# Kernel tuning notes

Hardware: AMD Instinct MI355X
Metric: run time of the kernel (lower is better)

## Reference

```python
import jax, jax.numpy as jnp
import numpy as np

N = 4096       # rows (batch * points)
D = 512        # d_model
H = 8          # num_heads


def setup_inputs() -> dict:
    key = jax.random.key(0)
    ks = jax.random.split(key, 11)
    s = 1.0 / np.sqrt(D).astype(np.float32)
    return {
        "x_q": jax.random.normal(ks[0], (N, D), jnp.float32),
        "x_k": jax.random.normal(ks[1], (N, D), jnp.float32),
        "x_v": jax.random.normal(ks[2], (N, D), jnp.float32),
        "Wq": jax.random.normal(ks[3], (D, D), jnp.float32) * s,
        "bq": jax.random.normal(ks[4], (D,), jnp.float32) * s,
        "Wk": jax.random.normal(ks[5], (D, D), jnp.float32) * s,
        "bk": jax.random.normal(ks[6], (D,), jnp.float32) * s,
        "Wv": jax.random.normal(ks[7], (D, D), jnp.float32) * s,
        "bv": jax.random.normal(ks[8], (D,), jnp.float32) * s,
        "Wo": jax.random.normal(ks[9], (D, D), jnp.float32) * s,
        "bo": jax.random.normal(ks[10], (D,), jnp.float32) * s,
    }


def reference(x_q, x_k, x_v, Wq, bq, Wk, bk, Wv, bv, Wo, bo):
    n, d = x_q.shape
    d_k = d // H
    # linear projections
    q = (x_q @ Wq + bq).reshape(n, H, d_k)  # chunk(dim=-1) == head split
    k = (x_k @ Wk + bk).reshape(n, H, d_k)
    v = (x_v @ Wv + bv).reshape(n, H, d_k)
    # channel-wise outer-product attention: scores[n,h,i,j] = q_i * k_j / sqrt(d_k)
    scale = jnp.asarray(1.0 / np.sqrt(d_k), q.dtype)
    scores = q[..., :, None] * k[..., None, :] * scale  # (n, H, d_k, d_k)
    p = jax.nn.softmax(scores, axis=-1)
    # attn output: p @ v over channel axis -> (n, H, d_k)
    x = jnp.einsum('nhij,nhj->nhi', p, v).reshape(n, d)  # head merge (cat dim=-1)
    return (x_q - x) @ Wo + bo
```

## Files before the change

kernel.cpp:

```cpp
#include <hip/hip_runtime.h>
#include <hip/hip_bf16.h>

#define NROWS 4096
#define DMODEL 512
#define NHEAD 8
#define DKH 64
#define ND (NROWS * DMODEL)
#define DD (DMODEL * DMODEL)

typedef unsigned short u16;
typedef __attribute__((ext_vector_type(8))) short short8;
typedef __attribute__((ext_vector_type(4))) float floatx4;

__device__ __forceinline__ u16 f2b(float f) {
    unsigned u = __float_as_uint(f);
    unsigned r = (u + 0x7fffu + ((u >> 16) & 1u)) >> 16;
    return (u16)r;
}
__device__ __forceinline__ float b2f(u16 v) {
    return __uint_as_float(((unsigned)v) << 16);
}
__device__ __forceinline__ void async16(const void* g, void* l) {
    __builtin_amdgcn_global_load_lds(g, l, 16, 0, 0);
}

__global__ __launch_bounds__(256) void convert_x(
    const float* __restrict__ s0, const float* __restrict__ s1,
    const float* __restrict__ s2, u16* __restrict__ d0, u16* __restrict__ d1,
    u16* __restrict__ d2, int nElem) {
    const float* s = blockIdx.z == 0 ? s0 : (blockIdx.z == 1 ? s1 : s2);
    u16* d = blockIdx.z == 0 ? d0 : (blockIdx.z == 1 ? d1 : d2);
    int i = (blockIdx.x * blockDim.x + threadIdx.x) * 4;
    if (i < nElem) {
        float4 v = *(const float4*)(s + i);
        ushort4 o;
        o.x = f2b(v.x); o.y = f2b(v.y); o.z = f2b(v.z); o.w = f2b(v.w);
        *(ushort4*)(d + i) = o;
    }
}

__global__ __launch_bounds__(256) void convert_w(
    const float* __restrict__ W0, const float* __restrict__ W1,
    const float* __restrict__ W2, const float* __restrict__ W3,
    u16* __restrict__ T0, u16* __restrict__ T1, u16* __restrict__ T2,
    u16* __restrict__ T3) {
    __shared__ float tile[32][33];
    int z = blockIdx.z;
    const float* W = z == 0 ? W0 : (z == 1 ? W1 : (z == 2 ? W2 : W3));
    u16* T = z == 0 ? T0 : (z == 1 ? T1 : (z == 2 ? T2 : T3));
    int n0 = blockIdx.x * 32, k0 = blockIdx.y * 32;
    int tx = threadIdx.x, ty = threadIdx.y;
#pragma unroll
    for (int r = 0; r < 32; r += 8)
        tile[ty + r][tx] = W[(size_t)(k0 + ty + r) * DMODEL + n0 + tx];
    __syncthreads();
#pragma unroll
    for (int r = 0; r < 32; r += 8) {
        int n = n0 + ty + r, k = k0 + tx;
        T[(size_t)n * DMODEL + k] = f2b(tile[tx][ty + r]);
    }
}

template <int OUTF>
__device__ __forceinline__ void gemm128_body(const u16* __restrict__ A,
                                             const u16* __restrict__ Bt,
                                             const float* __restrict__ bias,
                                             void* __restrict__ Cout) {
    __shared__ __align__(16) u16 lA[128 * 32];
    __shared__ __align__(16) u16 lB[128 * 32];
    const int tid = threadIdx.x;
    const int wave = tid >> 6, lane = tid & 63;
    const int tileM = blockIdx.y * 128;
    const int tileN = blockIdx.x * 128;
    const int wm = wave >> 1, wn = wave & 1;

    floatx4 acc[4][4];
#pragma unroll
    for (int i = 0; i < 4; i++)
#pragma unroll
        for (int j = 0; j < 4; j++) acc[i][j] = (floatx4){0.f, 0.f, 0.f, 0.f};

    const int lr4 = lane >> 2;
    const int ls = lane & 3;
    const int lrow = lane & 15;
    const int sk = lane >> 4;

    for (int t = 0; t < 16; ++t) {
        const int k0 = t * 32;
#pragma unroll
        for (int i = 0; i < 2; i++) {
            int c = wave * 2 + i;
            int r = c * 16 + lr4;
            int s = ls ^ ((r >> 1) & 3);
            async16(A + (size_t)(tileM + r) * 512 + k0 + s * 8, &lA[c * 512]);
            async16(Bt + (size_t)(tileN + r) * 512 + k0 + s * 8, &lB[c * 512]);
        }
        __syncthreads();

        short8 afr[4], bfr[4];
#pragma unroll
        for (int ni = 0; ni < 4; ++ni) {
            int r = wn * 64 + ni * 16 + lrow;
            int s = sk ^ ((r >> 1) & 3);
            bfr[ni] = *(const short8*)&lB[r * 32 + s * 8];
        }
#pragma unroll
        for (int mi = 0; mi < 4; ++mi) {
            int r = wm * 64 + mi * 16 + lrow;
            int s = sk ^ ((r >> 1) & 3);
            afr[mi] = *(const short8*)&lA[r * 32 + s * 8];
        }
#pragma unroll
        for (int mi = 0; mi < 4; ++mi)
#pragma unroll
            for (int ni = 0; ni < 4; ++ni)
                acc[mi][ni] = __builtin_amdgcn_mfma_f32_16x16x32_bf16(
                    afr[mi], bfr[ni], acc[mi][ni], 0, 0, 0);
        __syncthreads();
    }

#pragma unroll
    for (int mi = 0; mi < 4; ++mi) {
#pragma unroll
        for (int ni = 0; ni < 4; ++ni) {
            int col = tileN + wn * 64 + ni * 16 + lrow;
            float bv = bias[col];
#pragma unroll
            for (int r2 = 0; r2 < 4; r2++) {
                int row = tileM + wm * 64 + mi * 16 + sk * 4 + r2;
                float val = acc[mi][ni][r2] + bv;
                if (OUTF)
                    ((float*)Cout)[(size_t)row * 512 + col] = val;
                else
                    ((u16*)Cout)[(size_t)row * 512 + col] = f2b(val);
            }
        }
    }
}

__global__ __launch_bounds__(256) void proj3(
    const u16* __restrict__ xq, const u16* __restrict__ xk,
    const u16* __restrict__ xv, const u16* __restrict__ wtq,
    const u16* __restrict__ wtk, const u16* __restrict__ wtv,
    const float* __restrict__ bq, const float* __restrict__ bk,
    const float* __restrict__ bv, u16* __restrict__ Q, u16* __restrict__ K,
    u16* __restrict__ V) {
    int z = blockIdx.z;
    const u16* A = z == 0 ? xq : (z == 1 ? xk : xv);
    const u16* Bt = z == 0 ? wtq : (z == 1 ? wtk : wtv);
    const float* bias = z == 0 ? bq : (z == 1 ? bk : bv);
    u16* C = z == 0 ? Q : (z == 1 ? K : V);
    gemm128_body<0>(A, Bt, bias, C);
}

__global__ __launch_bounds__(256) void out_gemm(const u16* __restrict__ T,
                                                const u16* __restrict__ wto,
                                                const float* __restrict__ bo,
                                                float* __restrict__ C) {
    gemm128_body<1>(T, wto, bo, C);
}

__global__ __launch_bounds__(256) void attn_kernel(
    const u16* __restrict__ Qb, const u16* __restrict__ Kb,
    const u16* __restrict__ Vb, const float* __restrict__ xq,
    u16* __restrict__ Tout) {
    __shared__ float lk[4][64];
    __shared__ float lv[4][64];
    const int wave = threadIdx.x >> 6, lane = threadIdx.x & 63;
    const int p = blockIdx.x * 4 + wave;
    const int n = p >> 3, h = p & 7;
    const size_t base = (size_t)n * DMODEL + h * DKH;

    float q = b2f(Qb[base + lane]);
    lk[wave][lane] = b2f(Kb[base + lane]) * 0.125f;
    lv[wave][lane] = b2f(Vb[base + lane]);
    __syncthreads();

    float num = 0.f, den = 0.f;
#pragma unroll
    for (int j = 0; j < 64; j += 4) {
        float4 kv = *(const float4*)&lk[wave][j];
        float4 vv = *(const float4*)&lv[wave][j];
        float e0 = __expf(q * kv.x);
        float e1 = __expf(q * kv.y);
        float e2 = __expf(q * kv.z);
        float e3 = __expf(q * kv.w);
        den += e0 + e1 + e2 + e3;
        num += e0 * vv.x + e1 * vv.y + e2 * vv.z + e3 * vv.w;
    }
    float t = xq[base + lane] - num / den;
    Tout[base + lane] = f2b(t);
}

extern "C" void kernel_launch(void* const* d_in, const int* in_sizes, int n_in,
                              void* d_out, int out_size, void* d_ws,
                              size_t ws_size, hipStream_t stream) {
    const float* x_q = (const float*)d_in[0];
    const float* x_k = (const float*)d_in[1];
    const float* x_v = (const float*)d_in[2];
    const float* Wq = (const float*)d_in[3];
    const float* bq = (const float*)d_in[4];
    const float* Wk = (const float*)d_in[5];
    const float* bk = (const float*)d_in[6];
    const float* Wv = (const float*)d_in[7];
    const float* bv = (const float*)d_in[8];
    const float* Wo = (const float*)d_in[9];
    const float* bo = (const float*)d_in[10];

    u16* ws = (u16*)d_ws;
    u16* xqb = ws;
    u16* xkb = xqb + ND;
    u16* xvb = xkb + ND;
    u16* wtq = xvb + ND;
    u16* wtk = wtq + DD;
    u16* wtv = wtk + DD;
    u16* wto = wtv + DD;
    u16* Qb = wto + DD;
    u16* Kb = Qb + ND;
    u16* Vb = Kb + ND;
    u16* Tb = Vb + ND;

    convert_x<<<dim3(ND / 4 / 256, 1, 3), 256, 0, stream>>>(x_q, x_k, x_v, xqb,
                                                            xkb, xvb, ND);
    convert_w<<<dim3(16, 16, 4), dim3(32, 8), 0, stream>>>(Wq, Wk, Wv, Wo, wtq,
                                                           wtk, wtv, wto);
    proj3<<<dim3(DMODEL / 128, NROWS / 128, 3), 256, 0, stream>>>(
        xqb, xkb, xvb, wtq, wtk, wtv, bq, bk, bv, Qb, Kb, Vb);
    attn_kernel<<<dim3(NROWS * NHEAD / 4), 256, 0, stream>>>(Qb, Kb, Vb, x_q,
                                                             Tb);
    out_gemm<<<dim3(DMODEL / 128, NROWS / 128), 256, 0, stream>>>(
        Tb, wto, bo, (float*)d_out);
}
```

Baseline: 143.6 us.

## Fuse fp32-to-bf16 input conversion into projection GEMM with double-buffered 64x128 tiles

Removes the separate convert_x kernel. The projection GEMM now loads fp32 activations directly, converts them to bf16 in registers and writes them into LDS, which saves a full write and reread of three bf16 copies of the inputs. Both GEMMs switch to 64x128 tiles with double-buffered LDS so the next K-slice is prefetched while the current one feeds the MFMAs. They also use a 1D grid with an XCD-aware block remap to improve L2 locality and produce more blocks. The risks are extra register pressure from holding the prefetched fp32 values and less reuse per tile from the smaller M tile.

```diff
diff --git a/kernel.cpp b/kernel.cpp
--- a/kernel.cpp
+++ b/kernel.cpp
@@ -22,21 +22,6 @@
 }
 __device__ __forceinline__ void async16(const void* g, void* l) {
     __builtin_amdgcn_global_load_lds(g, l, 16, 0, 0);
-}
-
-__global__ __launch_bounds__(256) void convert_x(
-    const float* __restrict__ s0, const float* __restrict__ s1,
-    const float* __restrict__ s2, u16* __restrict__ d0, u16* __restrict__ d1,
-    u16* __restrict__ d2, int nElem) {
-    const float* s = blockIdx.z == 0 ? s0 : (blockIdx.z == 1 ? s1 : s2);
-    u16* d = blockIdx.z == 0 ? d0 : (blockIdx.z == 1 ? d1 : d2);
-    int i = (blockIdx.x * blockDim.x + threadIdx.x) * 4;
-    if (i < nElem) {
-        float4 v = *(const float4*)(s + i);
-        ushort4 o;
-        o.x = f2b(v.x); o.y = f2b(v.y); o.z = f2b(v.z); o.w = f2b(v.w);
-        *(ushort4*)(d + i) = o;
-    }
 }
 
 __global__ __launch_bounds__(256) void convert_w(
@@ -61,57 +46,207 @@
     }
 }
 
-template <int OUTF>
-__device__ __forceinline__ void gemm128_body(const u16* __restrict__ A,
-                                             const u16* __restrict__ Bt,
-                                             const float* __restrict__ bias,
-                                             void* __restrict__ Cout) {
-    __shared__ __align__(16) u16 lA[128 * 32];
-    __shared__ __align__(16) u16 lB[128 * 32];
+__global__ __launch_bounds__(256) void proj3(
+    const float* __restrict__ xq, const float* __restrict__ xk,
+    const float* __restrict__ xv, const u16* __restrict__ wtq,
+    const u16* __restrict__ wtk, const u16* __restrict__ wtv,
+    const float* __restrict__ bq, const float* __restrict__ bk,
+    const float* __restrict__ bv, u16* __restrict__ Q, u16* __restrict__ K,
+    u16* __restrict__ V) {
+    int d = blockIdx.x;
+    int id = (d & 7) * 96 + (d >> 3);
+    int z = id >> 8;
+    int t2 = id & 255;
+    const int tileM = (t2 >> 2) * 64;
+    const int tileN = (t2 & 3) * 128;
+
+    const float* A = z == 0 ? xq : (z == 1 ? xk : xv);
+    const u16* Bt = z == 0 ? wtq : (z == 1 ? wtk : wtv);
+    const float* bias = z == 0 ? bq : (z == 1 ? bk : bv);
+    u16* C = z == 0 ? Q : (z == 1 ? K : V);
+
+    __shared__ __align__(16) u16 lA[2][64 * 32];
+    __shared__ __align__(16) u16 lB[2][128 * 32];
+
     const int tid = threadIdx.x;
     const int wave = tid >> 6, lane = tid & 63;
-    const int tileM = blockIdx.y * 128;
-    const int tileN = blockIdx.x * 128;
     const int wm = wave >> 1, wn = wave & 1;
-
-    floatx4 acc[4][4];
-#pragma unroll
-    for (int i = 0; i < 4; i++)
+    const int lr4 = lane >> 2, ls = lane & 3;
+    const int lrow = lane & 15, sk = lane >> 4;
+
+    const int ar = tid >> 2;
+    const int asl = tid & 3;
+    const int asw = asl ^ ((ar >> 1) & 3);
+    const float* aptr = A + (size_t)(tileM + ar) * 512 + asl * 8;
+    u16* const awr0 = &lA[0][ar * 32 + asw * 8];
+    u16* const awr1 = &lA[1][ar * 32 + asw * 8];
+
+    int br0 = (wave * 2) * 16 + lr4;
+    int br1 = (wave * 2 + 1) * 16 + lr4;
+    int bs0 = ls ^ ((br0 >> 1) & 3);
+    int bs1 = ls ^ ((br1 >> 1) & 3);
+    const u16* bptr0 = Bt + (size_t)(tileN + br0) * 512 + bs0 * 8;
+    const u16* bptr1 = Bt + (size_t)(tileN + br1) * 512 + bs1 * 8;
+    u16* const bwr0_0 = &lB[0][(wave * 2) * 512];
+    u16* const bwr0_1 = &lB[0][(wave * 2 + 1) * 512];
+    u16* const bwr1_0 = &lB[1][(wave * 2) * 512];
+    u16* const bwr1_1 = &lB[1][(wave * 2 + 1) * 512];
+
+    floatx4 acc[2][4];
+#pragma unroll
+    for (int i = 0; i < 2; i++)
 #pragma unroll
         for (int j = 0; j < 4; j++) acc[i][j] = (floatx4){0.f, 0.f, 0.f, 0.f};
 
-    const int lr4 = lane >> 2;
-    const int ls = lane & 3;
-    const int lrow = lane & 15;
-    const int sk = lane >> 4;
+    async16(bptr0, bwr0_0);
+    async16(bptr1, bwr0_1);
+    {
+        float4 a0 = *(const float4*)aptr;
+        float4 a1 = *(const float4*)(aptr + 4);
+        short8 av;
+        av[0] = f2b(a0.x); av[1] = f2b(a0.y); av[2] = f2b(a0.z); av[3] = f2b(a0.w);
+        av[4] = f2b(a1.x); av[5] = f2b(a1.y); av[6] = f2b(a1.z); av[7] = f2b(a1.w);
+        *(short8*)awr0 = av;
+    }
+    __syncthreads();
 
     for (int t = 0; t < 16; ++t) {
-        const int k0 = t * 32;
-#pragma unroll
-        for (int i = 0; i < 2; i++) {
-            int c = wave * 2 + i;
-            int r = c * 16 + lr4;
-            int s = ls ^ ((r >> 1) & 3);
-            async16(A + (size_t)(tileM + r) * 512 + k0 + s * 8, &lA[c * 512]);
-            async16(Bt + (size_t)(tileN + r) * 512 + k0 + s * 8, &lB[c * 512]);
-        }
-        __syncthreads();
-
-        short8 afr[4], bfr[4];
+        const int cur = t & 1;
+        float4 na0, na1;
+        if (t < 15) {
+            const float* p = aptr + (t + 1) * 32;
+            na0 = *(const float4*)p;
+            na1 = *(const float4*)(p + 4);
+            const u16* q0 = bptr0 + (t + 1) * 32;
+            const u16* q1 = bptr1 + (t + 1) * 32;
+            if (cur == 0) {
+                async16(q0, bwr1_0);
+                async16(q1, bwr1_1);
+            } else {
+                async16(q0, bwr0_0);
+                async16(q1, bwr0_1);
+            }
+        }
+        short8 bfr[4], afr[2];
 #pragma unroll
         for (int ni = 0; ni < 4; ++ni) {
             int r = wn * 64 + ni * 16 + lrow;
             int s = sk ^ ((r >> 1) & 3);
-            bfr[ni] = *(const short8*)&lB[r * 32 + s * 8];
-        }
-#pragma unroll
-        for (int mi = 0; mi < 4; ++mi) {
-            int r = wm * 64 + mi * 16 + lrow;
+            bfr[ni] = *(const short8*)&lB[cur][r * 32 + s * 8];
+        }
+#pragma unroll
+        for (int mi = 0; mi < 2; ++mi) {
+            int r = wm * 32 + mi * 16 + lrow;
             int s = sk ^ ((r >> 1) & 3);
-            afr[mi] = *(const short8*)&lA[r * 32 + s * 8];
-        }
-#pragma unroll
-        for (int mi = 0; mi < 4; ++mi)
+            afr[mi] = *(const short8*)&lA[cur][r * 32 + s * 8];
+        }
+#pragma unroll
+        for (int mi = 0; mi < 2; ++mi)
+#pragma unroll
+            for (int ni = 0; ni < 4; ++ni)
+                acc[mi][ni] = __builtin_amdgcn_mfma_f32_16x16x32_bf16(
+                    afr[mi], bfr[ni], acc[mi][ni], 0, 0, 0);
+        if (t < 15) {
+            short8 av;
+            av[0] = f2b(na0.x); av[1] = f2b(na0.y); av[2] = f2b(na0.z); av[3] = f2b(na0.w);
+            av[4] = f2b(na1.x); av[5] = f2b(na1.y); av[6] = f2b(na1.z); av[7] = f2b(na1.w);
+            *(short8*)(cur == 0 ? awr1 : awr0) = av;
+        }
+        __syncthreads();
+    }
+
+#pragma unroll
+    for (int mi = 0; mi < 2; ++mi) {
+#pragma unroll
+        for (int ni = 0; ni < 4; ++ni) {
+            int col = tileN + wn * 64 + ni * 16 + lrow;
+            float bv = bias[col];
+#pragma unroll
+            for (int r2 = 0; r2 < 4; r2++) {
+                int row = tileM + wm * 32 + mi * 16 + sk * 4 + r2;
+                C[(size_t)row * 512 + col] = f2b(acc[mi][ni][r2] + bv);
+            }
+        }
+    }
+}
+
+__global__ __launch_bounds__(256) void out_gemm(const u16* __restrict__ T,
+                                                const u16* __restrict__ wto,
+                                                const float* __restrict__ bo,
+                                                float* __restrict__ C) {
+    int d = blockIdx.x;
+    int id = (d & 7) * 32 + (d >> 3);
+    const int tileM = (id >> 2) * 64;
+    const int tileN = (id & 3) * 128;
+
+    __shared__ __align__(16) u16 lA[2][64 * 32];
+    __shared__ __align__(16) u16 lB[2][128 * 32];
+
+    const int tid = threadIdx.x;
+    const int wave = tid >> 6, lane = tid & 63;
+    const int wm = wave >> 1, wn = wave & 1;
+    const int lr4 = lane >> 2, ls = lane & 3;
+    const int lrow = lane & 15, sk = lane >> 4;
+
+    int ar = wave * 16 + lr4;
+    int as = ls ^ ((ar >> 1) & 3);
+    const u16* aptr = T + (size_t)(tileM + ar) * 512 + as * 8;
+    u16* const awr0 = &lA[0][wave * 512];
+    u16* const awr1 = &lA[1][wave * 512];
+
+    int br0 = (wave * 2) * 16 + lr4;
+    int br1 = (wave * 2 + 1) * 16 + lr4;
+    int bs0 = ls ^ ((br0 >> 1) & 3);
+    int bs1 = ls ^ ((br1 >> 1) & 3);
+    const u16* bptr0 = wto + (size_t)(tileN + br0) * 512 + bs0 * 8;
+    const u16* bptr1 = wto + (size_t)(tileN + br1) * 512 + bs1 * 8;
+    u16* const bwr0_0 = &lB[0][(wave * 2) * 512];
+    u16* const bwr0_1 = &lB[0][(wave * 2 + 1) * 512];
+    u16* const bwr1_0 = &lB[1][(wave * 2) * 512];
+    u16* const bwr1_1 = &lB[1][(wave * 2 + 1) * 512];
+
+    floatx4 acc[2][4];
+#pragma unroll
+    for (int i = 0; i < 2; i++)
+#pragma unroll
+        for (int j = 0; j < 4; j++) acc[i][j] = (floatx4){0.f, 0.f, 0.f, 0.f};
+
+    async16(aptr, awr0);
+    async16(bptr0, bwr0_0);
+    async16(bptr1, bwr0_1);
+    __syncthreads();
+
+    for (int t = 0; t < 16; ++t) {
+        const int cur = t & 1;
+        if (t < 15) {
+            const u16* pa = aptr + (t + 1) * 32;
+            const u16* q0 = bptr0 + (t + 1) * 32;
+            const u16* q1 = bptr1 + (t + 1) * 32;
+            if (cur == 0) {
+                async16(pa, awr1);
+                async16(q0, bwr1_0);
+                async16(q1, bwr1_1);
+            } else {
+                async16(pa, awr0);
+                async16(q0, bwr0_0);
+                async16(q1, bwr0_1);
+            }
+        }
+        short8 bfr[4], afr[2];
+#pragma unroll
+        for (int ni = 0; ni < 4; ++ni) {
+            int r = wn * 64 + ni * 16 + lrow;
+            int s = sk ^ ((r >> 1) & 3);
+            bfr[ni] = *(const short8*)&lB[cur][r * 32 + s * 8];
+        }
+#pragma unroll
+        for (int mi = 0; mi < 2; ++mi) {
+            int r = wm * 32 + mi * 16 + lrow;
+            int s = sk ^ ((r >> 1) & 3);
+            afr[mi] = *(const short8*)&lA[cur][r * 32 + s * 8];
+        }
+#pragma unroll
+        for (int mi = 0; mi < 2; ++mi)
 #pragma unroll
             for (int ni = 0; ni < 4; ++ni)
                 acc[mi][ni] = __builtin_amdgcn_mfma_f32_16x16x32_bf16(
@@ -120,44 +255,18 @@
     }
 
 #pragma unroll
-    for (int mi = 0; mi < 4; ++mi) {
+    for (int mi = 0; mi < 2; ++mi) {
 #pragma unroll
         for (int ni = 0; ni < 4; ++ni) {
             int col = tileN + wn * 64 + ni * 16 + lrow;
-            float bv = bias[col];
+            float bv = bo[col];
 #pragma unroll
             for (int r2 = 0; r2 < 4; r2++) {
-                int row = tileM + wm * 64 + mi * 16 + sk * 4 + r2;
-                float val = acc[mi][ni][r2] + bv;
-                if (OUTF)
-                    ((float*)Cout)[(size_t)row * 512 + col] = val;
-                else
-                    ((u16*)Cout)[(size_t)row * 512 + col] = f2b(val);
+                int row = tileM + wm * 32 + mi * 16 + sk * 4 + r2;
+                C[(size_t)row * 512 + col] = acc[mi][ni][r2] + bv;
             }
         }
     }
-}
-
-__global__ __launch_bounds__(256) void proj3(
-    const u16* __restrict__ xq, const u16* __restrict__ xk,
-    const u16* __restrict__ xv, const u16* __restrict__ wtq,
-    const u16* __restrict__ wtk, const u16* __restrict__ wtv,
-    const float* __restrict__ bq, const float* __restrict__ bk,
-    const float* __restrict__ bv, u16* __restrict__ Q, u16* __restrict__ K,
-    u16* __restrict__ V) {
-    int z = blockIdx.z;
-    const u16* A = z == 0 ? xq : (z == 1 ? xk : xv);
-    const u16* Bt = z == 0 ? wtq : (z == 1 ? wtk : wtv);
-    const float* bias = z == 0 ? bq : (z == 1 ? bk : bv);
-    u16* C = z == 0 ? Q : (z == 1 ? K : V);
-    gemm128_body<0>(A, Bt, bias, C);
-}
-
-__global__ __launch_bounds__(256) void out_gemm(const u16* __restrict__ T,
-                                                const u16* __restrict__ wto,
-                                                const float* __restrict__ bo,
-                                                float* __restrict__ C) {
-    gemm128_body<1>(T, wto, bo, C);
 }
 
 __global__ __launch_bounds__(256) void attn_kernel(
@@ -208,10 +317,7 @@
     const float* bo = (const float*)d_in[10];
 
     u16* ws = (u16*)d_ws;
-    u16* xqb = ws;
-    u16* xkb = xqb + ND;
-    u16* xvb = xkb + ND;
-    u16* wtq = xvb + ND;
+    u16* wtq = ws;
     u16* wtk = wtq + DD;
     u16* wtv = wtk + DD;
     u16* wto = wtv + DD;
@@ -220,14 +326,11 @@
     u16* Vb = Kb + ND;
     u16* Tb = Vb + ND;
 
-    convert_x<<<dim3(ND / 4 / 256, 1, 3), 256, 0, stream>>>(x_q, x_k, x_v, xqb,
-                                                            xkb, xvb, ND);
     convert_w<<<dim3(16, 16, 4), dim3(32, 8), 0, stream>>>(Wq, Wk, Wv, Wo, wtq,
                                                            wtk, wtv, wto);
-    proj3<<<dim3(DMODEL / 128, NROWS / 128, 3), 256, 0, stream>>>(
-        xqb, xkb, xvb, wtq, wtk, wtv, bq, bk, bv, Qb, Kb, Vb);
+    proj3<<<dim3(768), 256, 0, stream>>>(x_q, x_k, x_v, wtq, wtk, wtv, bq, bk,
+                                         bv, Qb, Kb, Vb);
     attn_kernel<<<dim3(NROWS * NHEAD / 4), 256, 0, stream>>>(Qb, Kb, Vb, x_q,
                                                              Tb);
-    out_gemm<<<dim3(DMODEL / 128, NROWS / 128), 256, 0, stream>>>(
-        Tb, wto, bo, (float*)d_out);
-}
+    out_gemm<<<dim3(256), 256, 0, stream>>>(Tb, wto, bo, (float*)d_out);
+}
```

New measurement: 136.5 us. 1.05x faster.
